# Kernel tuning notes

Measured on AMD Instinct MI355X. Metric: run time of the kernel, lower is better.

The kernel has to match this reference:

```python
import jax, jax.numpy as jnp
import numpy as np


def setup_inputs() -> dict:
    key = jax.random.key(0)
    ks = jax.random.split(key, 6)
    B, T, S, E, D = 8, 128, 512, 512, 512  # batch, trg_len, src_len, enc_dim, trg_dim
    W_SCALE = 0.03  # small init to keep tanh unsaturated
    return {
        "hidden": jax.random.normal(ks[0], (B, T, D), jnp.float32),
        "encoder_outputs": jax.random.normal(ks[1], (B, S, E), jnp.float32),
        "encoder_mask": jnp.ones((B, S), jnp.float32),
        "W_attn": jax.random.normal(ks[2], (D, E + D), jnp.float32) * W_SCALE,
        "b_attn": jnp.zeros((D,), jnp.float32),
        "W_v": jax.random.normal(ks[3], (1, D), jnp.float32) * W_SCALE,
        "b_v": jnp.zeros((1,), jnp.float32),
        "W_out": jax.random.normal(ks[4], (D, E + D), jnp.float32) * W_SCALE,
    }


def masked_softmax(x, m, axis=-1):
    # faithful to repo: x*m, stable exp, e*m, normalize with eps
    x = x * m
    e_x = jnp.exp(x - jnp.max(x, axis=axis, keepdims=True))
    e_x = e_x * m
    return e_x / (jnp.sum(e_x, axis=axis, keepdims=True) + 1e-6)


def reference(hidden, encoder_outputs, encoder_mask, W_attn, b_attn, W_v, b_v, W_out):
    B, T, D = hidden.shape
    S = encoder_outputs.shape[1]
    # concat order in get_energy is (hidden_i, encoder_outputs), so split W_attn
    W_h = W_attn[:, :D]   # (D_out, trg_dim)
    W_e = W_attn[:, D:]   # (D_out, enc_dim)
    # Linear(concat) == h@W_h^T + e@W_e^T + b; vectorized over all (t, s) pairs
    hp = jnp.einsum('btd,kd->btk', hidden, W_h)            # (B,T,K)
    ep = jnp.einsum('bse,ke->bsk', encoder_outputs, W_e)   # (B,S,K)
    feat = jnp.tanh(hp[:, :, None, :] + ep[:, None, :, :] + b_attn)  # (B,T,S,K)
    energies = jnp.einsum('btsk,k->bts', feat, W_v[0]) + b_v[0]      # (B,T,S)
    # forward: energies * mask, then masked softmax
    m = encoder_mask[:, None, :]  # (B,1,S)
    energies = energies * m
    attn_weights = masked_softmax(energies, m, axis=-1)    # (B,T,S)
    weighted_context = jnp.einsum('bts,bse->bte', attn_weights, encoder_outputs)
    h_cat = jnp.concatenate([weighted_context, hidden], axis=-1)  # (B,T,E+D)
    h_tilde = jnp.tanh(jnp.einsum('btc,dc->btd', h_cat, W_out))   # (B,T,D)
    return h_tilde, weighted_context, attn_weights
```

## Files before the change

### kernel.cpp

```cpp
#include <hip/hip_runtime.h>
#include <hip/hip_bf16.h>
#include <math.h>

typedef unsigned short u16;
typedef unsigned int u32;
typedef __bf16 bf16x8 __attribute__((ext_vector_type(8)));
typedef float f32x4 __attribute__((ext_vector_type(4)));

#define OUT_WC   524288LL
#define OUT_ATTN 1048576LL
#define C2 2.8853900817779268f
#define LOG2E 1.4426950408889634f
#define LAS 40

__device__ inline u16 f2b(float f) {
    return (u16)((__float_as_uint(f) + 0x8000u) >> 16);
}
__device__ inline u32 pkcvt(float x, float y) {
    __hip_bfloat162 h = __float22bfloat162_rn(make_float2(x, y));
    return *(u32*)&h;
}
__device__ inline float tanh_fast(float x) {
    return 1.f - 2.f * __builtin_amdgcn_rcpf(__builtin_amdgcn_exp2f(C2 * x) + 1.f);
}

__global__ __launch_bounds__(256) void proj(
    const float* __restrict__ hidden, const float* __restrict__ enc,
    const float* __restrict__ Wattn, const float* __restrict__ battn,
    float* __restrict__ hp, u16* __restrict__ ept)
{
    __shared__ u16 lA[64 * LAS];
    __shared__ u16 lB[64 * LAS];
    const int tid = threadIdx.x;
    const int wvi = tid >> 6, ln = tid & 63;
    const int wm = wvi >> 1, wn = wvi & 1;
    const int l16 = ln & 15, quad = ln >> 4;
    const int blk = blockIdx.x;
    const bool ise = blk < 512;
    int bx, by, zz = 0, lda, ldb;
    const float *A, *B;
    if (ise) {
        zz = blk >> 6; by = (blk >> 3) & 7; bx = blk & 7;
        A = Wattn + 512; lda = 1024;
        B = enc + (long long)zz * 262144; ldb = 512;
    } else {
        int i = blk - 512; by = i >> 3; bx = i & 7;
        A = hidden; lda = 512;
        B = Wattn; ldb = 1024;
    }
    const int m0 = by * 64, n0 = bx * 64;
    const int srow = tid >> 2, skof = (tid & 3) * 8;
    const float* Ap = A + (long long)(m0 + srow) * lda + skof;
    const float* Bp = B + (long long)(n0 + srow) * ldb + skof;

    f32x4 acc00 = {0,0,0,0}, acc01 = {0,0,0,0}, acc10 = {0,0,0,0}, acc11 = {0,0,0,0};

    for (int k0 = 0; k0 < 512; k0 += 32) {
        float4 a0v = *(const float4*)(Ap + k0);
        float4 a1v = *(const float4*)(Ap + k0 + 4);
        float4 b0v = *(const float4*)(Bp + k0);
        float4 b1v = *(const float4*)(Bp + k0 + 4);
        __syncthreads();
        *(uint4*)&lA[srow * LAS + skof] =
            make_uint4(pkcvt(a0v.x,a0v.y), pkcvt(a0v.z,a0v.w), pkcvt(a1v.x,a1v.y), pkcvt(a1v.z,a1v.w));
        *(uint4*)&lB[srow * LAS + skof] =
            make_uint4(pkcvt(b0v.x,b0v.y), pkcvt(b0v.z,b0v.w), pkcvt(b1v.x,b1v.y), pkcvt(b1v.z,b1v.w));
        __syncthreads();
        bf16x8 a0 = *(const bf16x8*)&lA[(wm * 32      + l16) * LAS + quad * 8];
        bf16x8 a1 = *(const bf16x8*)&lA[(wm * 32 + 16 + l16) * LAS + quad * 8];
        bf16x8 b0 = *(const bf16x8*)&lB[(wn * 32      + l16) * LAS + quad * 8];
        bf16x8 b1 = *(const bf16x8*)&lB[(wn * 32 + 16 + l16) * LAS + quad * 8];
        acc00 = __builtin_amdgcn_mfma_f32_16x16x32_bf16(a0, b0, acc00, 0, 0, 0);
        acc01 = __builtin_amdgcn_mfma_f32_16x16x32_bf16(a0, b1, acc01, 0, 0, 0);
        acc10 = __builtin_amdgcn_mfma_f32_16x16x32_bf16(a1, b0, acc10, 0, 0, 0);
        acc11 = __builtin_amdgcn_mfma_f32_16x16x32_bf16(a1, b1, acc11, 0, 0, 0);
    }

    const f32x4* accs[4] = { &acc00, &acc01, &acc10, &acc11 };
    #pragma unroll
    for (int i = 0; i < 2; ++i) {
        #pragma unroll
        for (int j = 0; j < 2; ++j) {
            const f32x4& a = *accs[i * 2 + j];
            #pragma unroll
            for (int r = 0; r < 4; ++r) {
                int m = m0 + wm * 32 + i * 16 + quad * 4 + r;
                int n = n0 + wn * 32 + j * 16 + l16;
                float v = a[r];
                if (ise) ept[(long long)zz * 262144 + (long long)m * 512 + n] =
                             f2b(__builtin_amdgcn_exp2f(C2 * v));
                else     hp[(long long)m * 512 + n] = C2 * (v + battn[n]);
            }
        }
    }
}

template<int TANH, int BT>
__device__ inline void mm32_impl(
    const float* __restrict__ A1, const float* __restrict__ A2, int ksplit,
    int lda, long long strideA,
    const float* __restrict__ B_, int ldb, long long strideB,
    float* __restrict__ C_, int ldc, long long strideC, int K)
{
    __shared__ u16 lA[32 * LAS];
    __shared__ u16 lB[64 * LAS];
    const int tid = threadIdx.x;
    const int wvi = tid >> 6, ln = tid & 63;
    const int l16 = ln & 15, quad = ln >> 4;
    const int msub = wvi & 1, npair = wvi >> 1;
    const int m0 = blockIdx.y * 32, n0 = blockIdx.x * 64;
    const long long bz = blockIdx.z;
    const int rowA = tid >> 3, kofA = (tid & 7) * 4;
    const int rowB = tid >> 2, kofB = (tid & 3) * 8;
    const int tkrow = tid >> 3, tnof = (tid & 7) * 8;
    f32x4 acc0 = {0,0,0,0}, acc1 = {0,0,0,0};

    for (int k0 = 0; k0 < K; k0 += 32) {
        const float* Ap;
        if (k0 < ksplit) Ap = A1 + bz * strideA + (long long)(m0 + rowA) * lda + k0 + kofA;
        else             Ap = A2 + (long long)(m0 + rowA) * lda + (k0 - ksplit) + kofA;
        float4 av = *(const float4*)Ap;
        float4 bv0, bv1;
        if (!BT) {
            const float* Bp = B_ + bz * strideB + (long long)(n0 + rowB) * ldb + k0 + kofB;
            bv0 = *(const float4*)Bp; bv1 = *(const float4*)(Bp + 4);
        } else {
            const float* Bp = B_ + bz * strideB + (long long)(k0 + tkrow) * ldb + n0 + tnof;
            bv0 = *(const float4*)Bp; bv1 = *(const float4*)(Bp + 4);
        }
        __syncthreads();
        *(uint2*)&lA[rowA * LAS + kofA] = make_uint2(pkcvt(av.x, av.y), pkcvt(av.z, av.w));
        if (!BT) {
            int kk = kofB ^ (((rowB >> 3) & 3) << 3);
            *(uint4*)&lB[rowB * LAS + kk] =
                make_uint4(pkcvt(bv0.x,bv0.y), pkcvt(bv0.z,bv0.w), pkcvt(bv1.x,bv1.y), pkcvt(bv1.z,bv1.w));
        } else {
            #pragma unroll
            for (int i = 0; i < 8; ++i) {
                int n = tnof + i;
                int kk = tkrow ^ (((n >> 3) & 3) << 3);
                float val = (i < 4) ? ((const float*)&bv0)[i] : ((const float*)&bv1)[i - 4];
                lB[n * LAS + kk] = f2b(val);
            }
        }
        __syncthreads();
        bf16x8 a = *(const bf16x8*)&lA[(msub * 16 + l16) * LAS + quad * 8];
        int nr0 = npair * 32 + l16, nr1 = nr0 + 16;
        bf16x8 b0 = *(const bf16x8*)&lB[nr0 * LAS + (quad * 8 ^ (((nr0 >> 3) & 3) << 3))];
        bf16x8 b1 = *(const bf16x8*)&lB[nr1 * LAS + (quad * 8 ^ (((nr1 >> 3) & 3) << 3))];
        acc0 = __builtin_amdgcn_mfma_f32_16x16x32_bf16(a, b0, acc0, 0, 0, 0);
        acc1 = __builtin_amdgcn_mfma_f32_16x16x32_bf16(a, b1, acc1, 0, 0, 0);
    }
    #pragma unroll
    for (int j = 0; j < 2; ++j) {
        const f32x4& a = j ? acc1 : acc0;
        #pragma unroll
        for (int r = 0; r < 4; ++r) {
            int m = m0 + msub * 16 + quad * 4 + r;
            int n = n0 + npair * 32 + j * 16 + l16;
            float v = a[r];
            C_[bz * strideC + (long long)m * ldc + n] = TANH ? tanh_fast(v) : v;
        }
    }
}

#define MM32_ARGS const float* A1, const float* A2, int ksplit, int lda, \
    long long strideA, const float* B_, int ldb, long long strideB, \
    float* C_, int ldc, long long strideC, int K
#define MM32_PASS A1, A2, ksplit, lda, strideA, B_, ldb, strideB, C_, ldc, strideC, K
__global__ __launch_bounds__(256) void mm_wc  (MM32_ARGS) { mm32_impl<0, 1>(MM32_PASS); }
__global__ __launch_bounds__(256) void mm_hout(MM32_ARGS) { mm32_impl<1, 0>(MM32_PASS); }

__device__ inline float wred_sum(float v) {
    #pragma unroll
    for (int i = 32; i > 0; i >>= 1) v += __shfl_xor(v, i);
    return v;
}
__device__ inline float wred_max(float v) {
    #pragma unroll
    for (int i = 32; i > 0; i >>= 1) v = fmaxf(v, __shfl_xor(v, i));
    return v;
}
__device__ inline float bred_sum8(float v, float* red, int tid) {
    v = wred_sum(v);
    __syncthreads();
    if ((tid & 63) == 0) red[tid >> 6] = v;
    __syncthreads();
    float s = 0.f;
    #pragma unroll
    for (int i = 0; i < 8; ++i) s += red[i];
    return s;
}
__device__ inline float bred_max8(float v, float* red, int tid) {
    v = wred_max(v);
    __syncthreads();
    if ((tid & 63) == 0) red[tid >> 6] = v;
    __syncthreads();
    float s = red[0];
    #pragma unroll
    for (int i = 1; i < 8; ++i) s = fmaxf(s, red[i]);
    return s;
}

#define EN_STEP(c, j) { \
    float x0 = __uint_as_float((c) << 16); \
    float x1 = __uint_as_float((c) & 0xFFFF0000u); \
    float Hj = hk[kb + (j)]; \
    float wj = wk[kb + (j)]; \
    float s0 = wj * __builtin_amdgcn_rcpf(fmaf(Hj, x0, 1.f)); \
    float s1 = wj * __builtin_amdgcn_rcpf(fmaf(Hj, x1, 1.f)); \
    if ((j) & 1) { a0o += s0; a1o += s1; } else { a0e += s0; a1e += s1; } }

__global__ __launch_bounds__(512) void energies(
    const float* __restrict__ maskp, const float* __restrict__ hp,
    const u16* __restrict__ ept, const float* __restrict__ Wv,
    const float* __restrict__ bvp, float* __restrict__ attn)
{
    __shared__ __align__(16) float hp_s[512];
    __shared__ __align__(16) float wv_s[512];
    __shared__ float pa0[256], pa1[256];
    __shared__ float red[8];
    const int tid = threadIdx.x;
    const int b = blockIdx.x >> 7;
    const int t = blockIdx.x & 127;

    float w = Wv[tid];
    wv_s[tid] = w;
    hp_s[tid] = __builtin_amdgcn_exp2f(hp[(long long)(b * 128 + t) * 512 + tid]);
    float sumWv = bred_sum8(w, red, tid);

    const int kh = tid >> 8, sp = tid & 255;
    const float* __restrict__ hk = &hp_s[kh * 256];
    const float* __restrict__ wk = &wv_s[kh * 256];
    const u16* eb = ept + (long long)b * 262144 + kh * 131072 + 2 * sp;

    float a0e = 0.f, a0o = 0.f, a1e = 0.f, a1o = 0.f;
    u32 c0, c1, c2, c3, c4, c5, c6, c7;
    c0 = *(const u32*)(eb);            c1 = *(const u32*)(eb + 512);
    c2 = *(const u32*)(eb + 1024);     c3 = *(const u32*)(eb + 1536);
    c4 = *(const u32*)(eb + 2048);     c5 = *(const u32*)(eb + 2560);
    c6 = *(const u32*)(eb + 3072);     c7 = *(const u32*)(eb + 3584);
    for (int kb = 0; kb < 248; kb += 8) {
        const u16* nb = eb + (kb + 8) * 512;
        u32 n0v = *(const u32*)(nb);           u32 n1v = *(const u32*)(nb + 512);
        u32 n2v = *(const u32*)(nb + 1024);    u32 n3v = *(const u32*)(nb + 1536);
        u32 n4v = *(const u32*)(nb + 2048);    u32 n5v = *(const u32*)(nb + 2560);
        u32 n6v = *(const u32*)(nb + 3072);    u32 n7v = *(const u32*)(nb + 3584);
        EN_STEP(c0, 0) EN_STEP(c1, 1) EN_STEP(c2, 2) EN_STEP(c3, 3)
        EN_STEP(c4, 4) EN_STEP(c5, 5) EN_STEP(c6, 6) EN_STEP(c7, 7)
        c0 = n0v; c1 = n1v; c2 = n2v; c3 = n3v;
        c4 = n4v; c5 = n5v; c6 = n6v; c7 = n7v;
    }
    { const int kb = 248;
      EN_STEP(c0, 0) EN_STEP(c1, 1) EN_STEP(c2, 2) EN_STEP(c3, 3)
      EN_STEP(c4, 4) EN_STEP(c5, 5) EN_STEP(c6, 6) EN_STEP(c7, 7) }
    float a0 = a0e + a0o, a1 = a1e + a1o;

    if (kh) { pa0[sp] = a0; pa1[sp] = a1; }
    __syncthreads();
    float r0 = -1e30f, r1 = -1e30f, mv0 = 0.f, mv1 = 0.f;
    if (!kh) {
        a0 += pa0[sp]; a1 += pa1[sp];
        float bv0 = bvp[0];
        float2 mv = *(const float2*)(maskp + (long long)b * 512 + 2 * sp);
        mv0 = mv.x; mv1 = mv.y;
        r0 = (bv0 + sumWv - 2.f * a0) * mv0; r0 *= mv0;
        r1 = (bv0 + sumWv - 2.f * a1) * mv1; r1 *= mv1;
    }
    float mx = bred_max8(fmaxf(r0, r1), red, tid);
    float ex0 = 0.f, ex1 = 0.f;
    if (!kh) {
        ex0 = __builtin_amdgcn_exp2f((r0 - mx) * LOG2E) * mv0;
        ex1 = __builtin_amdgcn_exp2f((r1 - mx) * LOG2E) * mv1;
    }
    float sm = bred_sum8(ex0 + ex1, red, tid);
    if (!kh) {
        float inv = 1.f / (sm + 1e-6f);
        float2 o = make_float2(ex0 * inv, ex1 * inv);
        *(float2*)(attn + (long long)(b * 128 + t) * 512 + 2 * sp) = o;
    }
}

extern "C" void kernel_launch(void* const* d_in, const int* in_sizes, int n_in,
                              void* d_out, int out_size, void* d_ws, size_t ws_size,
                              hipStream_t stream)
{
    const float* hidden = (const float*)d_in[0];
    const float* enc    = (const float*)d_in[1];
    const float* mask   = (const float*)d_in[2];
    const float* Wattn  = (const float*)d_in[3];
    const float* battn  = (const float*)d_in[4];
    const float* Wv     = (const float*)d_in[5];
    const float* bvp    = (const float*)d_in[6];
    const float* Wout   = (const float*)d_in[7];
    float* out = (float*)d_out;

    float* hp = (float*)d_ws;
    u16*   ept = (u16*)((char*)d_ws + (2 << 20));

    proj<<<640, 256, 0, stream>>>(hidden, enc, Wattn, battn, hp, ept);
    energies<<<1024, 512, 0, stream>>>(mask, hp, ept, Wv, bvp, out + OUT_ATTN);
    mm_wc<<<dim3(8, 4, 8), 256, 0, stream>>>(
        out + OUT_ATTN, out + OUT_ATTN, 1 << 30, 512, 65536,
        enc, 512, 262144, out + OUT_WC, 512, 65536, 512);
    mm_hout<<<dim3(8, 32, 1), 256, 0, stream>>>(
        out + OUT_WC, hidden, 512, 512, 0,
        Wout, 1024, 0, out, 512, 0, 1024);
}
```

Before: 165.4 us.

## Process two target rows per energies block with 8-wide k-split and vectorized loads

The energies kernel now computes two target timesteps per block, so each bf16 encoder-projection load is reused for both rows. The K dimension is split across 8 wavefront groups, each thread handles 8 source positions with 16-byte loads, and partial sums are reduced through a larger shared buffer. Exp(hp) and Wv are packed into one float4 shared entry, and the softmax reductions are batched for both rows. This halves global traffic on ept and launches half as many blocks. The cost is more registers per thread and 32KB of shared memory, which may lower occupancy.

Measured after the change: 151.9 us. 1.09x faster.

```diff
diff --git a/kernel.cpp b/kernel.cpp
--- a/kernel.cpp
+++ b/kernel.cpp
@@ -176,11 +176,6 @@
     for (int i = 32; i > 0; i >>= 1) v += __shfl_xor(v, i);
     return v;
 }
-__device__ inline float wred_max(float v) {
-    #pragma unroll
-    for (int i = 32; i > 0; i >>= 1) v = fmaxf(v, __shfl_xor(v, i));
-    return v;
-}
 __device__ inline float bred_sum8(float v, float* red, int tid) {
     v = wred_sum(v);
     __syncthreads();
@@ -191,94 +186,119 @@
     for (int i = 0; i < 8; ++i) s += red[i];
     return s;
 }
-__device__ inline float bred_max8(float v, float* red, int tid) {
-    v = wred_max(v);
-    __syncthreads();
-    if ((tid & 63) == 0) red[tid >> 6] = v;
-    __syncthreads();
-    float s = red[0];
-    #pragma unroll
-    for (int i = 1; i < 8; ++i) s = fmaxf(s, red[i]);
-    return s;
-}
-
-#define EN_STEP(c, j) { \
-    float x0 = __uint_as_float((c) << 16); \
-    float x1 = __uint_as_float((c) & 0xFFFF0000u); \
-    float Hj = hk[kb + (j)]; \
-    float wj = wk[kb + (j)]; \
-    float s0 = wj * __builtin_amdgcn_rcpf(fmaf(Hj, x0, 1.f)); \
-    float s1 = wj * __builtin_amdgcn_rcpf(fmaf(Hj, x1, 1.f)); \
-    if ((j) & 1) { a0o += s0; a1o += s1; } else { a0e += s0; a1e += s1; } }
+__device__ inline void bred2_max(float v0, float v1, float* red, int tid,
+                                 float* o0, float* o1) {
+    #pragma unroll
+    for (int i = 32; i > 0; i >>= 1) {
+        v0 = fmaxf(v0, __shfl_xor(v0, i));
+        v1 = fmaxf(v1, __shfl_xor(v1, i));
+    }
+    __syncthreads();
+    if ((tid & 63) == 0) { red[tid >> 6] = v0; red[8 + (tid >> 6)] = v1; }
+    __syncthreads();
+    float a0 = red[0], a1 = red[8];
+    #pragma unroll
+    for (int i = 1; i < 8; ++i) { a0 = fmaxf(a0, red[i]); a1 = fmaxf(a1, red[8 + i]); }
+    *o0 = a0; *o1 = a1;
+}
+__device__ inline void bred2_sum(float v0, float v1, float* red, int tid,
+                                 float* o0, float* o1) {
+    #pragma unroll
+    for (int i = 32; i > 0; i >>= 1) { v0 += __shfl_xor(v0, i); v1 += __shfl_xor(v1, i); }
+    __syncthreads();
+    if ((tid & 63) == 0) { red[tid >> 6] = v0; red[8 + (tid >> 6)] = v1; }
+    __syncthreads();
+    float a0 = 0.f, a1 = 0.f;
+    #pragma unroll
+    for (int i = 0; i < 8; ++i) { a0 += red[i]; a1 += red[8 + i]; }
+    *o0 = a0; *o1 = a1;
+}
+
+__device__ inline void proc8(uint4 c, float4 hw, float* a0, float* a1) {
+    u32 cc[4] = {c.x, c.y, c.z, c.w};
+    #pragma unroll
+    for (int i = 0; i < 4; ++i) {
+        float xl = __uint_as_float(cc[i] << 16);
+        float xh = __uint_as_float(cc[i] & 0xFFFF0000u);
+        float rl0 = __builtin_amdgcn_rcpf(fmaf(hw.x, xl, 1.f));
+        float rh0 = __builtin_amdgcn_rcpf(fmaf(hw.x, xh, 1.f));
+        float rl1 = __builtin_amdgcn_rcpf(fmaf(hw.y, xl, 1.f));
+        float rh1 = __builtin_amdgcn_rcpf(fmaf(hw.y, xh, 1.f));
+        a0[2*i]   = fmaf(hw.z, rl0, a0[2*i]);
+        a0[2*i+1] = fmaf(hw.z, rh0, a0[2*i+1]);
+        a1[2*i]   = fmaf(hw.z, rl1, a1[2*i]);
+        a1[2*i+1] = fmaf(hw.z, rh1, a1[2*i+1]);
+    }
+}
 
 __global__ __launch_bounds__(512) void energies(
     const float* __restrict__ maskp, const float* __restrict__ hp,
     const u16* __restrict__ ept, const float* __restrict__ Wv,
     const float* __restrict__ bvp, float* __restrict__ attn)
 {
-    __shared__ __align__(16) float hp_s[512];
-    __shared__ __align__(16) float wv_s[512];
-    __shared__ float pa0[256], pa1[256];
-    __shared__ float red[8];
+    __shared__ __align__(16) float4 hpw[512];
+    __shared__ float pa[2][8][512];
+    __shared__ float red[16];
     const int tid = threadIdx.x;
-    const int b = blockIdx.x >> 7;
-    const int t = blockIdx.x & 127;
+    const int b = blockIdx.x >> 6;
+    const int t0 = (blockIdx.x & 63) * 2;
 
     float w = Wv[tid];
-    wv_s[tid] = w;
-    hp_s[tid] = __builtin_amdgcn_exp2f(hp[(long long)(b * 128 + t) * 512 + tid]);
+    float h0 = hp[(long long)(b * 128 + t0) * 512 + tid];
+    float h1 = hp[(long long)(b * 128 + t0 + 1) * 512 + tid];
+    hpw[tid] = make_float4(__builtin_amdgcn_exp2f(h0), __builtin_amdgcn_exp2f(h1), w, 0.f);
     float sumWv = bred_sum8(w, red, tid);
 
-    const int kh = tid >> 8, sp = tid & 255;
-    const float* __restrict__ hk = &hp_s[kh * 256];
-    const float* __restrict__ wk = &wv_s[kh * 256];
-    const u16* eb = ept + (long long)b * 262144 + kh * 131072 + 2 * sp;
-
-    float a0e = 0.f, a0o = 0.f, a1e = 0.f, a1o = 0.f;
-    u32 c0, c1, c2, c3, c4, c5, c6, c7;
-    c0 = *(const u32*)(eb);            c1 = *(const u32*)(eb + 512);
-    c2 = *(const u32*)(eb + 1024);     c3 = *(const u32*)(eb + 1536);
-    c4 = *(const u32*)(eb + 2048);     c5 = *(const u32*)(eb + 2560);
-    c6 = *(const u32*)(eb + 3072);     c7 = *(const u32*)(eb + 3584);
-    for (int kb = 0; kb < 248; kb += 8) {
-        const u16* nb = eb + (kb + 8) * 512;
-        u32 n0v = *(const u32*)(nb);           u32 n1v = *(const u32*)(nb + 512);
-        u32 n2v = *(const u32*)(nb + 1024);    u32 n3v = *(const u32*)(nb + 1536);
-        u32 n4v = *(const u32*)(nb + 2048);    u32 n5v = *(const u32*)(nb + 2560);
-        u32 n6v = *(const u32*)(nb + 3072);    u32 n7v = *(const u32*)(nb + 3584);
-        EN_STEP(c0, 0) EN_STEP(c1, 1) EN_STEP(c2, 2) EN_STEP(c3, 3)
-        EN_STEP(c4, 4) EN_STEP(c5, 5) EN_STEP(c6, 6) EN_STEP(c7, 7)
-        c0 = n0v; c1 = n1v; c2 = n2v; c3 = n3v;
-        c4 = n4v; c5 = n5v; c6 = n6v; c7 = n7v;
-    }
-    { const int kb = 248;
-      EN_STEP(c0, 0) EN_STEP(c1, 1) EN_STEP(c2, 2) EN_STEP(c3, 3)
-      EN_STEP(c4, 4) EN_STEP(c5, 5) EN_STEP(c6, 6) EN_STEP(c7, 7) }
-    float a0 = a0e + a0o, a1 = a1e + a1o;
-
-    if (kh) { pa0[sp] = a0; pa1[sp] = a1; }
-    __syncthreads();
-    float r0 = -1e30f, r1 = -1e30f, mv0 = 0.f, mv1 = 0.f;
-    if (!kh) {
-        a0 += pa0[sp]; a1 += pa1[sp];
-        float bv0 = bvp[0];
-        float2 mv = *(const float2*)(maskp + (long long)b * 512 + 2 * sp);
-        mv0 = mv.x; mv1 = mv.y;
-        r0 = (bv0 + sumWv - 2.f * a0) * mv0; r0 *= mv0;
-        r1 = (bv0 + sumWv - 2.f * a1) * mv1; r1 *= mv1;
-    }
-    float mx = bred_max8(fmaxf(r0, r1), red, tid);
-    float ex0 = 0.f, ex1 = 0.f;
-    if (!kh) {
-        ex0 = __builtin_amdgcn_exp2f((r0 - mx) * LOG2E) * mv0;
-        ex1 = __builtin_amdgcn_exp2f((r1 - mx) * LOG2E) * mv1;
-    }
-    float sm = bred_sum8(ex0 + ex1, red, tid);
-    if (!kh) {
-        float inv = 1.f / (sm + 1e-6f);
-        float2 o = make_float2(ex0 * inv, ex1 * inv);
-        *(float2*)(attn + (long long)(b * 128 + t) * 512 + 2 * sp) = o;
-    }
+    const int kg = tid >> 6, sl = tid & 63;
+    const int s0 = sl * 8;
+    const u16* eb = ept + (long long)b * 262144 + (kg * 64) * 512 + s0;
+    const float4* hq = &hpw[kg * 64];
+
+    float a0[8] = {0,0,0,0,0,0,0,0}, a1[8] = {0,0,0,0,0,0,0,0};
+    uint4 c0 = *(const uint4*)(eb);
+    uint4 c1 = *(const uint4*)(eb + 512);
+    uint4 c2 = *(const uint4*)(eb + 1024);
+    uint4 c3 = *(const uint4*)(eb + 1536);
+    for (int kk = 0; kk < 60; kk += 4) {
+        const u16* nb = eb + (kk + 4) * 512;
+        uint4 n0 = *(const uint4*)(nb);
+        uint4 n1 = *(const uint4*)(nb + 512);
+        uint4 n2 = *(const uint4*)(nb + 1024);
+        uint4 n3 = *(const uint4*)(nb + 1536);
+        proc8(c0, hq[kk],     a0, a1);
+        proc8(c1, hq[kk + 1], a0, a1);
+        proc8(c2, hq[kk + 2], a0, a1);
+        proc8(c3, hq[kk + 3], a0, a1);
+        c0 = n0; c1 = n1; c2 = n2; c3 = n3;
+    }
+    proc8(c0, hq[60], a0, a1);
+    proc8(c1, hq[61], a0, a1);
+    proc8(c2, hq[62], a0, a1);
+    proc8(c3, hq[63], a0, a1);
+
+    *(float4*)&pa[0][kg][s0]     = make_float4(a0[0], a0[1], a0[2], a0[3]);
+    *(float4*)&pa[0][kg][s0 + 4] = make_float4(a0[4], a0[5], a0[6], a0[7]);
+    *(float4*)&pa[1][kg][s0]     = make_float4(a1[0], a1[1], a1[2], a1[3]);
+    *(float4*)&pa[1][kg][s0 + 4] = make_float4(a1[4], a1[5], a1[6], a1[7]);
+    __syncthreads();
+
+    const int s = tid;
+    float A0 = 0.f, A1 = 0.f;
+    #pragma unroll
+    for (int g = 0; g < 8; ++g) { A0 += pa[0][g][s]; A1 += pa[1][g][s]; }
+    float mv = maskp[(long long)b * 512 + s];
+    float bv0 = bvp[0];
+    float r0 = (bv0 + sumWv - 2.f * A0) * mv; r0 *= mv;
+    float r1 = (bv0 + sumWv - 2.f * A1) * mv; r1 *= mv;
+
+    float mx0, mx1;
+    bred2_max(r0, r1, red, tid, &mx0, &mx1);
+    float ex0 = __builtin_amdgcn_exp2f((r0 - mx0) * LOG2E) * mv;
+    float ex1 = __builtin_amdgcn_exp2f((r1 - mx1) * LOG2E) * mv;
+    float sm0, sm1;
+    bred2_sum(ex0, ex1, red, tid, &sm0, &sm1);
+    attn[(long long)(b * 128 + t0) * 512 + s]     = ex0 * (1.f / (sm0 + 1e-6f));
+    attn[(long long)(b * 128 + t0 + 1) * 512 + s] = ex1 * (1.f / (sm1 + 1e-6f));
 }
 
 extern "C" void kernel_launch(void* const* d_in, const int* in_sizes, int n_in,
@@ -299,7 +319,7 @@
     u16*   ept = (u16*)((char*)d_ws + (2 << 20));
 
     proj<<<640, 256, 0, stream>>>(hidden, enc, Wattn, battn, hp, ept);
-    energies<<<1024, 512, 0, stream>>>(mask, hp, ept, Wv, bvp, out + OUT_ATTN);
+    energies<<<512, 512, 0, stream>>>(mask, hp, ept, Wv, bvp, out + OUT_ATTN);
     mm_wc<<<dim3(8, 4, 8), 256, 0, stream>>>(
         out + OUT_ATTN, out + OUT_ATTN, 1 << 30, 512, 65536,
         enc, 512, 262144, out + OUT_WC, 512, 65536, 512);
```
